# Optimization experiments

Measured on AMD Instinct MI355X. Metric: run time of the kernel, lower is better.

## Reference

```python
import jax, jax.numpy as jnp
import numpy as np

NUM_ITEMS = 50000
NUM_USERS = 16384   # static number of user segments (total_user universe)
H0 = 512            # encoder_hidden_size[0]
LAT = 256           # bottleneck (encoder_hidden_size[-1] / decoder_hidden_size[0])
N = 262144          # observed interactions
NT = 262144         # target interactions


def setup_inputs() -> dict:
    key = jax.random.key(0)
    ks = jax.random.split(key, 14)

    def glorot(k, shape):
        fan_in, fan_out = shape[1], shape[0]
        lim = np.sqrt(6.0 / (fan_in + fan_out)).astype(np.float32)
        return jax.random.uniform(k, shape, jnp.float32, -lim, lim)

    return {
        "user": jax.random.randint(ks[0], (N,), 0, NUM_USERS, jnp.int32),
        "item": jax.random.randint(ks[1], (N,), 0, NUM_ITEMS, jnp.int32),
        "rating": jax.random.normal(ks[2], (N,), jnp.float32),
        "target_user": jax.random.randint(ks[3], (NT,), 0, NUM_USERS, jnp.int32),
        "target_item": jax.random.randint(ks[4], (NT,), 0, NUM_ITEMS, jnp.int32),
        "target_rating": jax.random.normal(ks[5], (NT,), jnp.float32),
        # encoder_linear: Linear(num_items, H0)
        "W_enc": glorot(ks[6], (H0, NUM_ITEMS)),
        "b_enc": jnp.zeros((H0,), jnp.float32),
        # Encoder: Linear(H0, LAT) + Tanh
        "W1": glorot(ks[7], (LAT, H0)),
        "b1": jnp.zeros((LAT,), jnp.float32),
        # Decoder: Linear(LAT, H0) + Tanh
        "W2": glorot(ks[8], (H0, LAT)),
        "b2": jnp.zeros((H0,), jnp.float32),
        # decoder_linear: Linear(H0, num_items)
        "W_dec": glorot(ks[9], (NUM_ITEMS, H0)),
        "b_dec": jnp.zeros((NUM_ITEMS,), jnp.float32),
    }


def reference(user, item, rating, target_user, target_item, target_rating,
              W_enc, b_enc, W1, b1, W2, b2, W_dec, b_dec):
    # --- encoder: gather item weight rows, scale by rating, segment-sum per user ---
    # rows: [N, H0] gather from W_enc.T ([NUM_ITEMS, H0])
    rows = W_enc.T[item] * rating[:, None]
    # per-user aggregation over the full user universe (equivalent to the
    # torch unique/sort/index_add path: users with no interactions get 0 -> tanh(bias))
    agg = jax.ops.segment_sum(rows, user, num_segments=NUM_USERS)  # [U, H0]
    x = jnp.tanh(agg + b_enc)
    # --- small dense tanh MLP encoder/decoder ---
    encoded = jnp.tanh(x @ W1.T + b1)          # [U, LAT]
    decoded = jnp.tanh(encoded @ W2.T + b2)    # [U, H0] (dropout = identity, eval mode)
    # --- decoder: gather user codes & item decoder rows, rowwise dot ---
    g = decoded[target_user]                   # [NT, H0]
    w = W_dec[target_item]                     # [NT, H0]
    pred = jnp.sum(g * w, axis=-1) + b_dec[target_item]  # [NT]
    loss = jnp.mean((pred - target_rating) ** 2)
    return pred, loss
```

## Files before the change

kernel.cpp:

```cpp
#include <hip/hip_runtime.h>
#include <hip/hip_bf16.h>
#include <math.h>

#define NUM_ITEMS 50000
#define NUM_USERS 16384
#define ITEM_BINS 50176
#define H0 512
#define LAT 256

typedef __attribute__((ext_vector_type(8))) short short8;
typedef __attribute__((ext_vector_type(4))) float floatx4;

__device__ __forceinline__ unsigned short f2bf(float f) {
    union { float f; unsigned i; } u; u.f = f;
    unsigned r = u.i + 0x7fff + ((u.i >> 16) & 1);
    return (unsigned short)(r >> 16);
}
__device__ __forceinline__ float bfhi(unsigned v) {
    union { unsigned i; float f; } u; u.i = v & 0xffff0000u; return u.f;
}
__device__ __forceinline__ float bflo(unsigned v) {
    union { unsigned i; float f; } u; u.i = v << 16; return u.f;
}

__global__ void transpose_kernel(const float* __restrict__ src, unsigned short* __restrict__ dst) {
    __shared__ float tile[32][33];
    int tx = threadIdx.x, ty = threadIdx.y;
    int x0 = blockIdx.x * 32, y0 = blockIdx.y * 32;
    int x = x0 + tx;
    if (x < NUM_ITEMS) {
#pragma unroll
        for (int j = 0; j < 32; j += 8)
            tile[ty + j][tx] = src[(size_t)(y0 + ty + j) * NUM_ITEMS + x];
    }
    __syncthreads();
#pragma unroll
    for (int j = 0; j < 32; j += 8) {
        int it = x0 + ty + j;
        if (it < NUM_ITEMS)
            dst[(size_t)it * H0 + y0 + tx] = f2bf(tile[tx][ty + j]);
    }
}

__global__ void f2bf2_kernel(const float* __restrict__ a, unsigned short* __restrict__ da,
                             const float* __restrict__ b, unsigned short* __restrict__ db, int n) {
    int i = blockIdx.x * blockDim.x + threadIdx.x;
    if (i < n) da[i] = f2bf(a[i]);
    else { int j = i - n; if (j < n) db[j] = f2bf(b[j]); }
}

__global__ void count_kernel(const int* __restrict__ user, int* __restrict__ cntU,
                             const int* __restrict__ t_item, int* __restrict__ cntI,
                             int n, int nt) {
    int i = blockIdx.x * blockDim.x + threadIdx.x;
    if (i < n) atomicAdd(&cntU[user[i]], 1);
    if (i < nt) atomicAdd(&cntI[t_item[i]], 1);
}

__device__ void scan_block(const int* __restrict__ cnt, int* __restrict__ offs,
                           int* __restrict__ cursor, int per) {
    __shared__ int ssum[1024];
    int t = threadIdx.x;
    int base = t * per;
    int s = 0;
    for (int j = 0; j < per; ++j) s += cnt[base + j];
    ssum[t] = s;
    __syncthreads();
    for (int off = 1; off < 1024; off <<= 1) {
        int v = (t >= off) ? ssum[t - off] : 0;
        __syncthreads();
        ssum[t] += v;
        __syncthreads();
    }
    int run = (t == 0) ? 0 : ssum[t - 1];
    for (int j = 0; j < per; ++j) {
        offs[base + j] = run;
        cursor[base + j] = run;
        run += cnt[base + j];
    }
}

__global__ void scan_kernel(const int* __restrict__ cntU, int* __restrict__ offsU, int* __restrict__ curU,
                            const int* __restrict__ cntI, int* __restrict__ offsI, int* __restrict__ curI) {
    if (blockIdx.x == 0) scan_block(cntU, offsU, curU, NUM_USERS / 1024);
    else scan_block(cntI, offsI, curI, ITEM_BINS / 1024);
}

__global__ void scatter_kernel(const int* __restrict__ user, const int* __restrict__ item,
                               const float* __restrict__ rating, int* __restrict__ curU,
                               int* __restrict__ s_item, float* __restrict__ s_rat,
                               const int* __restrict__ t_user, const int* __restrict__ t_item,
                               const float* __restrict__ t_rating, int* __restrict__ curI,
                               int* __restrict__ st_user, int* __restrict__ st_item,
                               float* __restrict__ st_rat, int* __restrict__ st_idx,
                               int n, int nt) {
    int i = blockIdx.x * blockDim.x + threadIdx.x;
    if (i < n) {
        int u = user[i];
        int pos = atomicAdd(&curU[u], 1);
        s_item[pos] = item[i];
        s_rat[pos] = rating[i];
    }
    if (i < nt) {
        int it = t_item[i];
        int pos = atomicAdd(&curI[it], 1);
        st_user[pos] = t_user[i];
        st_item[pos] = it;
        st_rat[pos] = t_rating[i];
        st_idx[pos] = i;
    }
}

__global__ __launch_bounds__(256) void agg_kernel(const unsigned short* __restrict__ wtb,
                                                  const int* __restrict__ offs,
                                                  const int* __restrict__ ends,
                                                  const int* __restrict__ s_item,
                                                  const float* __restrict__ s_rat,
                                                  const float* __restrict__ b_enc,
                                                  unsigned short* __restrict__ xb) {
    __shared__ float red[3 * 512];
    int u = blockIdx.x;
    int tid = threadIdx.x;
    int g = tid >> 6, lane = tid & 63;
    float acc[8] = {};
    int j0 = offs[u], j1 = ends[u];
    for (int j = j0 + g; j < j1; j += 4) {
        int it = s_item[j];
        float r = s_rat[j];
        uint4 v = ((const uint4*)(wtb + (size_t)it * H0))[lane];
        acc[0] += bflo(v.x) * r; acc[1] += bfhi(v.x) * r;
        acc[2] += bflo(v.y) * r; acc[3] += bfhi(v.y) * r;
        acc[4] += bflo(v.z) * r; acc[5] += bfhi(v.z) * r;
        acc[6] += bflo(v.w) * r; acc[7] += bfhi(v.w) * r;
    }
    if (g) {
        float4* rp = (float4*)red + (size_t)(g - 1) * 128 + lane * 2;
        rp[0] = make_float4(acc[0], acc[1], acc[2], acc[3]);
        rp[1] = make_float4(acc[4], acc[5], acc[6], acc[7]);
    }
    __syncthreads();
    if (g == 0) {
#pragma unroll
        for (int h = 0; h < 3; ++h) {
            const float* rp = red + h * 512 + lane * 8;
#pragma unroll
            for (int e = 0; e < 8; ++e) acc[e] += rp[e];
        }
        float4 b0 = ((const float4*)b_enc)[lane * 2];
        float4 b1 = ((const float4*)b_enc)[lane * 2 + 1];
        unsigned short o[8];
        o[0] = f2bf(tanhf(acc[0] + b0.x)); o[1] = f2bf(tanhf(acc[1] + b0.y));
        o[2] = f2bf(tanhf(acc[2] + b0.z)); o[3] = f2bf(tanhf(acc[3] + b0.w));
        o[4] = f2bf(tanhf(acc[4] + b1.x)); o[5] = f2bf(tanhf(acc[5] + b1.y));
        o[6] = f2bf(tanhf(acc[6] + b1.z)); o[7] = f2bf(tanhf(acc[7] + b1.w));
        uint4 pk;
        pk.x = (unsigned)o[0] | ((unsigned)o[1] << 16);
        pk.y = (unsigned)o[2] | ((unsigned)o[3] << 16);
        pk.z = (unsigned)o[4] | ((unsigned)o[5] << 16);
        pk.w = (unsigned)o[6] | ((unsigned)o[7] << 16);
        ((uint4*)(xb + (size_t)u * H0))[lane] = pk;
    }
}

__global__ __launch_bounds__(256) void gemm_mfma(const unsigned short* __restrict__ A,
                                                 const unsigned short* __restrict__ B,
                                                 const float* __restrict__ bias,
                                                 unsigned short* __restrict__ C,
                                                 int Nn, int K) {
    __shared__ unsigned short Ash[128 * 32];
    __shared__ unsigned short Bsh[128 * 32];
    int tid = threadIdx.x;
    int wid = tid >> 6, lane = tid & 63;
    int wave_m = wid & 1, wave_n = wid >> 1;
    int quad = lane >> 4, l16 = lane & 15;
    int m0 = blockIdx.x * 128, n0 = blockIdx.y * 128;
    floatx4 acc[4][4] = {};

    int srow = lane >> 2;
    int scol = (lane & 3) * 8;
    for (int k0 = 0; k0 < K; k0 += 32) {
#pragma unroll
        for (int i = 0; i < 2; ++i) {
            int c = wid * 2 + i;
            int row = c * 16 + srow;
            const unsigned short* ga = A + (size_t)(m0 + row) * K + k0 + scol;
            const unsigned short* gb = B + (size_t)(n0 + row) * K + k0 + scol;
            __builtin_amdgcn_global_load_lds(
                (const __attribute__((address_space(1))) void*)ga,
                (__attribute__((address_space(3))) void*)((__attribute__((address_space(3))) char*)Ash + c * 1024),
                16, 0, 0);
            __builtin_amdgcn_global_load_lds(
                (const __attribute__((address_space(1))) void*)gb,
                (__attribute__((address_space(3))) void*)((__attribute__((address_space(3))) char*)Bsh + c * 1024),
                16, 0, 0);
        }
        __syncthreads();
        short8 af[4], bfr[4];
#pragma unroll
        for (int i = 0; i < 4; ++i) {
            int ml = wave_m * 64 + i * 16 + l16;
            af[i] = ((const short8*)Ash)[ml * 4 + quad];
            int nl = wave_n * 64 + i * 16 + l16;
            bfr[i] = ((const short8*)Bsh)[nl * 4 + quad];
        }
#pragma unroll
        for (int i = 0; i < 4; ++i)
#pragma unroll
            for (int j = 0; j < 4; ++j)
                acc[i][j] = __builtin_amdgcn_mfma_f32_16x16x32_bf16(af[i], bfr[j], acc[i][j], 0, 0, 0);
        __syncthreads();
    }
#pragma unroll
    for (int j = 0; j < 4; ++j) {
        int col = n0 + wave_n * 64 + j * 16 + l16;
        float bv = bias[col];
#pragma unroll
        for (int i = 0; i < 4; ++i) {
            int rowb = m0 + wave_m * 64 + i * 16 + quad * 4;
#pragma unroll
            for (int r = 0; r < 4; ++r)
                C[(size_t)(rowb + r) * Nn + col] = f2bf(tanhf(acc[i][j][r] + bv));
        }
    }
}

__global__ __launch_bounds__(256) void predict_kernel(const unsigned short* __restrict__ dec_b,
                                                      const float* __restrict__ W_dec,
                                                      const float* __restrict__ b_dec,
                                                      const int* __restrict__ st_user,
                                                      const int* __restrict__ st_item,
                                                      const float* __restrict__ st_rat,
                                                      const int* __restrict__ st_idx,
                                                      float* __restrict__ pred,
                                                      float* __restrict__ partials, int NT) {
    __shared__ float wsum[4];
    int wid = threadIdx.x >> 6, lane = threadIdx.x & 63;
    int base = (blockIdx.x * 4 + wid) * 4;
    float sq = 0.f;
    int tu[4], ti[4];
    uint4 gv[4];
    float4 wv0[4], wv1[4];
#pragma unroll
    for (int t = 0; t < 4; ++t) {
        int idx = min(base + t, NT - 1);
        tu[t] = st_user[idx];
        ti[t] = st_item[idx];
    }
#pragma unroll
    for (int t = 0; t < 4; ++t) {
        gv[t] = ((const uint4*)(dec_b + (size_t)tu[t] * H0))[lane];
        const float4* w = (const float4*)(W_dec + (size_t)ti[t] * H0);
        wv0[t] = w[lane * 2];
        wv1[t] = w[lane * 2 + 1];
    }
#pragma unroll
    for (int t = 0; t < 4; ++t) {
        float s = bflo(gv[t].x) * wv0[t].x + bfhi(gv[t].x) * wv0[t].y
                + bflo(gv[t].y) * wv0[t].z + bfhi(gv[t].y) * wv0[t].w
                + bflo(gv[t].z) * wv1[t].x + bfhi(gv[t].z) * wv1[t].y
                + bflo(gv[t].w) * wv1[t].z + bfhi(gv[t].w) * wv1[t].w;
#pragma unroll
        for (int off = 32; off; off >>= 1) s += __shfl_xor(s, off, 64);
        if (lane == 0 && base + t < NT) {
            int idx = base + t;
            float p = s + b_dec[ti[t]];
            pred[st_idx[idx]] = p;
            float d = p - st_rat[idx];
            sq += d * d;
        }
    }
    if (lane == 0) wsum[wid] = sq;
    __syncthreads();
    if (threadIdx.x == 0) partials[blockIdx.x] = wsum[0] + wsum[1] + wsum[2] + wsum[3];
}

__global__ void loss_reduce(const float* __restrict__ partials, float* __restrict__ out_loss,
                            int nPart, float invNT) {
    __shared__ float s[256];
    int t = threadIdx.x;
    float a = 0.f;
    for (int i = t; i < nPart; i += 256) a += partials[i];
    s[t] = a;
    __syncthreads();
    for (int off = 128; off; off >>= 1) {
        if (t < off) s[t] += s[t + off];
        __syncthreads();
    }
    if (t == 0) out_loss[0] = s[0] * invNT;
}

extern "C" void kernel_launch(void* const* d_in, const int* in_sizes, int n_in,
                              void* d_out, int out_size, void* d_ws, size_t ws_size,
                              hipStream_t stream) {
    const int* user = (const int*)d_in[0];
    const int* item = (const int*)d_in[1];
    const float* rating = (const float*)d_in[2];
    const int* t_user = (const int*)d_in[3];
    const int* t_item = (const int*)d_in[4];
    const float* t_rating = (const float*)d_in[5];
    const float* W_enc = (const float*)d_in[6];
    const float* b_enc = (const float*)d_in[7];
    const float* W1 = (const float*)d_in[8];
    const float* b1 = (const float*)d_in[9];
    const float* W2 = (const float*)d_in[10];
    const float* b2 = (const float*)d_in[11];
    const float* W_dec = (const float*)d_in[12];
    const float* b_dec = (const float*)d_in[13];
    const int N = in_sizes[0];
    const int NT = in_sizes[3];

    char* ws = (char*)d_ws;
    size_t off = 0;
    auto alloc = [&](size_t bytes) {
        void* p = ws + off;
        off = (off + bytes + 255) & ~(size_t)255;
        return p;
    };
    unsigned short* wtb = (unsigned short*)alloc((size_t)NUM_ITEMS * H0 * 2);
    unsigned short* xb = (unsigned short*)alloc((size_t)NUM_USERS * H0 * 2);
    unsigned short* enc_b = (unsigned short*)alloc((size_t)NUM_USERS * LAT * 2);
    unsigned short* dec_b = (unsigned short*)alloc((size_t)NUM_USERS * H0 * 2);
    unsigned short* w1b = (unsigned short*)alloc((size_t)LAT * H0 * 2);
    unsigned short* w2b = (unsigned short*)alloc((size_t)H0 * LAT * 2);
    int* cntU = (int*)alloc((size_t)(NUM_USERS + ITEM_BINS) * 4);
    int* cntI = cntU + NUM_USERS;
    int* offsU = (int*)alloc((size_t)NUM_USERS * 4);
    int* curU = (int*)alloc((size_t)NUM_USERS * 4);
    int* offsI = (int*)alloc((size_t)ITEM_BINS * 4);
    int* curI = (int*)alloc((size_t)ITEM_BINS * 4);
    int* s_item = (int*)alloc((size_t)N * 4);
    float* s_rat = (float*)alloc((size_t)N * 4);
    int* st_user = (int*)alloc((size_t)NT * 4);
    int* st_item = (int*)alloc((size_t)NT * 4);
    float* st_rat = (float*)alloc((size_t)NT * 4);
    int* st_idx = (int*)alloc((size_t)NT * 4);
    const int predBlocks = (NT + 15) / 16;
    float* partials = (float*)alloc((size_t)predBlocks * 4);

    float* pred = (float*)d_out;
    float* loss = pred + NT;

    const int maxNNT = N > NT ? N : NT;
    hipMemsetAsync(cntU, 0, (size_t)(NUM_USERS + ITEM_BINS) * 4, stream);
    count_kernel<<<(maxNNT + 255) / 256, 256, 0, stream>>>(user, cntU, t_item, cntI, N, NT);
    scan_kernel<<<2, 1024, 0, stream>>>(cntU, offsU, curU, cntI, offsI, curI);
    scatter_kernel<<<(maxNNT + 255) / 256, 256, 0, stream>>>(
        user, item, rating, curU, s_item, s_rat,
        t_user, t_item, t_rating, curI, st_user, st_item, st_rat, st_idx, N, NT);
    transpose_kernel<<<dim3((NUM_ITEMS + 31) / 32, H0 / 32), dim3(32, 8), 0, stream>>>(W_enc, wtb);
    f2bf2_kernel<<<(2 * LAT * H0 + 255) / 256, 256, 0, stream>>>(W1, w1b, W2, w2b, LAT * H0);
    agg_kernel<<<NUM_USERS, 256, 0, stream>>>(wtb, offsU, curU, s_item, s_rat, b_enc, xb);
    gemm_mfma<<<dim3(NUM_USERS / 128, LAT / 128), 256, 0, stream>>>(xb, w1b, b1, enc_b, LAT, H0);
    gemm_mfma<<<dim3(NUM_USERS / 128, H0 / 128), 256, 0, stream>>>(enc_b, w2b, b2, dec_b, H0, LAT);
    predict_kernel<<<predBlocks, 256, 0, stream>>>(dec_b, W_dec, b_dec, st_user, st_item, st_rat,
                                                   st_idx, pred, partials, NT);
    loss_reduce<<<1, 256, 0, stream>>>(partials, loss, predBlocks, 1.0f / NT);
}
```

Before: 472.8 us.

## Fuse setup kernels, pack sorted records, convert W_dec to bf16, shrink GEMM tile

Merges the W_enc transpose, weight conversions and counting into one multi-role setup kernel with wider 64x64 transpose tiles and vectorized count loads. Sorted interaction and target records are packed into int2/int4 structs so each needs one load, and the agg loop prefetches the next record. W_dec is converted to bf16 up front so predict gathers half the bytes, at the cost of a full extra streaming pass over W_dec and lower precision in the dot product. The GEMM is templated to a 128x64 tile for more blocks, and the scan and loss reduce use vector loads.

```diff
diff --git a/kernel.cpp b/kernel.cpp
--- a/kernel.cpp
+++ b/kernel.cpp
@@ -4,7 +4,7 @@
 
 #define NUM_ITEMS 50000
 #define NUM_USERS 16384
-#define ITEM_BINS 50176
+#define ITEM_BINS 65536
 #define H0 512
 #define LAT 256
 
@@ -22,39 +22,76 @@
 __device__ __forceinline__ float bflo(unsigned v) {
     union { unsigned i; float f; } u; u.i = v << 16; return u.f;
 }
-
-__global__ void transpose_kernel(const float* __restrict__ src, unsigned short* __restrict__ dst) {
-    __shared__ float tile[32][33];
-    int tx = threadIdx.x, ty = threadIdx.y;
-    int x0 = blockIdx.x * 32, y0 = blockIdx.y * 32;
-    int x = x0 + tx;
-    if (x < NUM_ITEMS) {
-#pragma unroll
-        for (int j = 0; j < 32; j += 8)
-            tile[ty + j][tx] = src[(size_t)(y0 + ty + j) * NUM_ITEMS + x];
-    }
-    __syncthreads();
-#pragma unroll
-    for (int j = 0; j < 32; j += 8) {
-        int it = x0 + ty + j;
-        if (it < NUM_ITEMS)
-            dst[(size_t)it * H0 + y0 + tx] = f2bf(tile[tx][ty + j]);
-    }
-}
-
-__global__ void f2bf2_kernel(const float* __restrict__ a, unsigned short* __restrict__ da,
-                             const float* __restrict__ b, unsigned short* __restrict__ db, int n) {
-    int i = blockIdx.x * blockDim.x + threadIdx.x;
-    if (i < n) da[i] = f2bf(a[i]);
-    else { int j = i - n; if (j < n) db[j] = f2bf(b[j]); }
-}
-
-__global__ void count_kernel(const int* __restrict__ user, int* __restrict__ cntU,
-                             const int* __restrict__ t_item, int* __restrict__ cntI,
-                             int n, int nt) {
-    int i = blockIdx.x * blockDim.x + threadIdx.x;
-    if (i < n) atomicAdd(&cntU[user[i]], 1);
-    if (i < nt) atomicAdd(&cntI[t_item[i]], 1);
+__device__ __forceinline__ uint4 pack8(const float* v) {
+    uint4 p;
+    p.x = (unsigned)f2bf(v[0]) | ((unsigned)f2bf(v[1]) << 16);
+    p.y = (unsigned)f2bf(v[2]) | ((unsigned)f2bf(v[3]) << 16);
+    p.z = (unsigned)f2bf(v[4]) | ((unsigned)f2bf(v[5]) << 16);
+    p.w = (unsigned)f2bf(v[6]) | ((unsigned)f2bf(v[7]) << 16);
+    return p;
+}
+
+__global__ __launch_bounds__(256) void setup_kernel(
+        const float* __restrict__ W_enc, unsigned short* __restrict__ wtb,
+        const float* __restrict__ W_dec, unsigned short* __restrict__ wdb,
+        const float* __restrict__ W1, unsigned short* __restrict__ w1b,
+        const float* __restrict__ W2, unsigned short* __restrict__ w2b,
+        const int* __restrict__ user, int* __restrict__ cntU,
+        const int* __restrict__ t_item, int* __restrict__ cntI,
+        int n, int nt, int TB, int DB, int CB) {
+    __shared__ float tile[64][65];
+    int bid = blockIdx.x;
+    int tid = threadIdx.x;
+    if (bid < TB) {
+        const int TBX = (NUM_ITEMS + 63) / 64;
+        int bx = bid % TBX, by = bid / TBX;
+        int x0 = bx * 64, y0 = by * 64;
+        int tx = tid & 63, ty = tid >> 6;
+        int x = x0 + tx;
+        if (x < NUM_ITEMS) {
+#pragma unroll
+            for (int j = 0; j < 64; j += 4)
+                tile[j + ty][tx] = W_enc[(size_t)(y0 + j + ty) * NUM_ITEMS + x];
+        }
+        __syncthreads();
+#pragma unroll
+        for (int j = 0; j < 64; j += 4) {
+            int it = x0 + j + ty;
+            if (it < NUM_ITEMS)
+                wtb[(size_t)it * H0 + y0 + tx] = f2bf(tile[tx][j + ty]);
+        }
+    } else if (bid < TB + DB) {
+        int idx = (bid - TB) * 2048 + tid * 8;
+        float v[8];
+        *(float4*)&v[0] = *(const float4*)(W_dec + idx);
+        *(float4*)&v[4] = *(const float4*)(W_dec + idx + 4);
+        *(uint4*)(wdb + idx) = pack8(v);
+    } else if (bid < TB + DB + CB) {
+        int i = (bid - TB - DB) * 1024 + tid * 4;
+        if (i + 3 < n) {
+            int4 u = *(const int4*)(user + i);
+            atomicAdd(&cntU[u.x], 1); atomicAdd(&cntU[u.y], 1);
+            atomicAdd(&cntU[u.z], 1); atomicAdd(&cntU[u.w], 1);
+        } else {
+            for (int k = i; k < n; ++k) atomicAdd(&cntU[user[k]], 1);
+        }
+        if (i + 3 < nt) {
+            int4 t = *(const int4*)(t_item + i);
+            atomicAdd(&cntI[t.x], 1); atomicAdd(&cntI[t.y], 1);
+            atomicAdd(&cntI[t.z], 1); atomicAdd(&cntI[t.w], 1);
+        } else {
+            for (int k = i; k < nt; ++k) atomicAdd(&cntI[t_item[k]], 1);
+        }
+    } else {
+        int b2i = bid - TB - DB - CB;
+        const float* src = (b2i < 64) ? W1 : W2;
+        unsigned short* dst = (b2i < 64) ? w1b : w2b;
+        int idx = (b2i & 63) * 2048 + tid * 8;
+        float v[8];
+        *(float4*)&v[0] = *(const float4*)(src + idx);
+        *(float4*)&v[4] = *(const float4*)(src + idx + 4);
+        *(uint4*)(dst + idx) = pack8(v);
+    }
 }
 
 __device__ void scan_block(const int* __restrict__ cnt, int* __restrict__ offs,
@@ -63,7 +100,10 @@
     int t = threadIdx.x;
     int base = t * per;
     int s = 0;
-    for (int j = 0; j < per; ++j) s += cnt[base + j];
+    for (int j = 0; j < per; j += 4) {
+        int4 v = *(const int4*)(cnt + base + j);
+        s += v.x + v.y + v.z + v.w;
+    }
     ssum[t] = s;
     __syncthreads();
     for (int off = 1; off < 1024; off <<= 1) {
@@ -73,10 +113,15 @@
         __syncthreads();
     }
     int run = (t == 0) ? 0 : ssum[t - 1];
-    for (int j = 0; j < per; ++j) {
-        offs[base + j] = run;
-        cursor[base + j] = run;
-        run += cnt[base + j];
+    for (int j = 0; j < per; j += 4) {
+        int4 v = *(const int4*)(cnt + base + j);
+        int4 o;
+        o.x = run; run += v.x;
+        o.y = run; run += v.y;
+        o.z = run; run += v.z;
+        o.w = run; run += v.w;
+        *(int4*)(offs + base + j) = o;
+        *(int4*)(cursor + base + j) = o;
     }
 }
 
@@ -88,34 +133,27 @@
 
 __global__ void scatter_kernel(const int* __restrict__ user, const int* __restrict__ item,
                                const float* __restrict__ rating, int* __restrict__ curU,
-                               int* __restrict__ s_item, float* __restrict__ s_rat,
+                               int2* __restrict__ s_pack,
                                const int* __restrict__ t_user, const int* __restrict__ t_item,
                                const float* __restrict__ t_rating, int* __restrict__ curI,
-                               int* __restrict__ st_user, int* __restrict__ st_item,
-                               float* __restrict__ st_rat, int* __restrict__ st_idx,
-                               int n, int nt) {
+                               int4* __restrict__ st_pack, int n, int nt) {
     int i = blockIdx.x * blockDim.x + threadIdx.x;
     if (i < n) {
         int u = user[i];
         int pos = atomicAdd(&curU[u], 1);
-        s_item[pos] = item[i];
-        s_rat[pos] = rating[i];
+        s_pack[pos] = make_int2(item[i], __float_as_int(rating[i]));
     }
     if (i < nt) {
         int it = t_item[i];
         int pos = atomicAdd(&curI[it], 1);
-        st_user[pos] = t_user[i];
-        st_item[pos] = it;
-        st_rat[pos] = t_rating[i];
-        st_idx[pos] = i;
+        st_pack[pos] = make_int4(t_user[i], it, __float_as_int(t_rating[i]), i);
     }
 }
 
 __global__ __launch_bounds__(256) void agg_kernel(const unsigned short* __restrict__ wtb,
                                                   const int* __restrict__ offs,
                                                   const int* __restrict__ ends,
-                                                  const int* __restrict__ s_item,
-                                                  const float* __restrict__ s_rat,
+                                                  const int2* __restrict__ s_pack,
                                                   const float* __restrict__ b_enc,
                                                   unsigned short* __restrict__ xb) {
     __shared__ float red[3 * 512];
@@ -124,14 +162,19 @@
     int g = tid >> 6, lane = tid & 63;
     float acc[8] = {};
     int j0 = offs[u], j1 = ends[u];
-    for (int j = j0 + g; j < j1; j += 4) {
-        int it = s_item[j];
-        float r = s_rat[j];
-        uint4 v = ((const uint4*)(wtb + (size_t)it * H0))[lane];
+    int j = j0 + g;
+    int2 nxt = (j < j1) ? s_pack[j] : make_int2(0, 0);
+    while (j < j1) {
+        int2 cur = nxt;
+        int jn = j + 4;
+        if (jn < j1) nxt = s_pack[jn];
+        float r = __int_as_float(cur.y);
+        uint4 v = ((const uint4*)(wtb + (size_t)cur.x * H0))[lane];
         acc[0] += bflo(v.x) * r; acc[1] += bfhi(v.x) * r;
         acc[2] += bflo(v.y) * r; acc[3] += bfhi(v.y) * r;
         acc[4] += bflo(v.z) * r; acc[5] += bfhi(v.z) * r;
         acc[6] += bflo(v.w) * r; acc[7] += bfhi(v.w) * r;
+        j = jn;
     }
     if (g) {
         float4* rp = (float4*)red + (size_t)(g - 1) * 128 + lane * 2;
@@ -148,71 +191,74 @@
         }
         float4 b0 = ((const float4*)b_enc)[lane * 2];
         float4 b1 = ((const float4*)b_enc)[lane * 2 + 1];
-        unsigned short o[8];
-        o[0] = f2bf(tanhf(acc[0] + b0.x)); o[1] = f2bf(tanhf(acc[1] + b0.y));
-        o[2] = f2bf(tanhf(acc[2] + b0.z)); o[3] = f2bf(tanhf(acc[3] + b0.w));
-        o[4] = f2bf(tanhf(acc[4] + b1.x)); o[5] = f2bf(tanhf(acc[5] + b1.y));
-        o[6] = f2bf(tanhf(acc[6] + b1.z)); o[7] = f2bf(tanhf(acc[7] + b1.w));
-        uint4 pk;
-        pk.x = (unsigned)o[0] | ((unsigned)o[1] << 16);
-        pk.y = (unsigned)o[2] | ((unsigned)o[3] << 16);
-        pk.z = (unsigned)o[4] | ((unsigned)o[5] << 16);
-        pk.w = (unsigned)o[6] | ((unsigned)o[7] << 16);
-        ((uint4*)(xb + (size_t)u * H0))[lane] = pk;
-    }
-}
-
+        float o[8];
+        o[0] = tanhf(acc[0] + b0.x); o[1] = tanhf(acc[1] + b0.y);
+        o[2] = tanhf(acc[2] + b0.z); o[3] = tanhf(acc[3] + b0.w);
+        o[4] = tanhf(acc[4] + b1.x); o[5] = tanhf(acc[5] + b1.y);
+        o[6] = tanhf(acc[6] + b1.z); o[7] = tanhf(acc[7] + b1.w);
+        ((uint4*)(xb + (size_t)u * H0))[lane] = pack8(o);
+    }
+}
+
+template<int BN>
 __global__ __launch_bounds__(256) void gemm_mfma(const unsigned short* __restrict__ A,
                                                  const unsigned short* __restrict__ B,
                                                  const float* __restrict__ bias,
                                                  unsigned short* __restrict__ C,
                                                  int Nn, int K) {
+    constexpr int WN = BN / 32;
+    constexpr int NCH = 8 + BN / 16;
+    constexpr int PER = NCH / 4;
     __shared__ unsigned short Ash[128 * 32];
-    __shared__ unsigned short Bsh[128 * 32];
+    __shared__ unsigned short Bsh[BN * 32];
     int tid = threadIdx.x;
     int wid = tid >> 6, lane = tid & 63;
     int wave_m = wid & 1, wave_n = wid >> 1;
     int quad = lane >> 4, l16 = lane & 15;
-    int m0 = blockIdx.x * 128, n0 = blockIdx.y * 128;
-    floatx4 acc[4][4] = {};
-
+    int m0 = blockIdx.x * 128, n0 = blockIdx.y * BN;
+    floatx4 acc[4][WN] = {};
     int srow = lane >> 2;
     int scol = (lane & 3) * 8;
     for (int k0 = 0; k0 < K; k0 += 32) {
 #pragma unroll
-        for (int i = 0; i < 2; ++i) {
-            int c = wid * 2 + i;
-            int row = c * 16 + srow;
-            const unsigned short* ga = A + (size_t)(m0 + row) * K + k0 + scol;
-            const unsigned short* gb = B + (size_t)(n0 + row) * K + k0 + scol;
-            __builtin_amdgcn_global_load_lds(
-                (const __attribute__((address_space(1))) void*)ga,
-                (__attribute__((address_space(3))) void*)((__attribute__((address_space(3))) char*)Ash + c * 1024),
-                16, 0, 0);
-            __builtin_amdgcn_global_load_lds(
-                (const __attribute__((address_space(1))) void*)gb,
-                (__attribute__((address_space(3))) void*)((__attribute__((address_space(3))) char*)Bsh + c * 1024),
-                16, 0, 0);
-        }
-        __syncthreads();
-        short8 af[4], bfr[4];
+        for (int i = 0; i < PER; ++i) {
+            int c = wid * PER + i;
+            if (c < 8) {
+                const unsigned short* ga = A + (size_t)(m0 + c * 16 + srow) * K + k0 + scol;
+                __builtin_amdgcn_global_load_lds(
+                    (const __attribute__((address_space(1))) void*)ga,
+                    (__attribute__((address_space(3))) void*)((__attribute__((address_space(3))) char*)Ash + c * 1024),
+                    16, 0, 0);
+            } else {
+                const unsigned short* gb = B + (size_t)(n0 + (c - 8) * 16 + srow) * K + k0 + scol;
+                __builtin_amdgcn_global_load_lds(
+                    (const __attribute__((address_space(1))) void*)gb,
+                    (__attribute__((address_space(3))) void*)((__attribute__((address_space(3))) char*)Bsh + (c - 8) * 1024),
+                    16, 0, 0);
+            }
+        }
+        __syncthreads();
+        short8 af[4], bfr[WN];
 #pragma unroll
         for (int i = 0; i < 4; ++i) {
             int ml = wave_m * 64 + i * 16 + l16;
             af[i] = ((const short8*)Ash)[ml * 4 + quad];
-            int nl = wave_n * 64 + i * 16 + l16;
-            bfr[i] = ((const short8*)Bsh)[nl * 4 + quad];
+        }
+#pragma unroll
+        for (int j = 0; j < WN; ++j) {
+            int nl = wave_n * (BN / 2) + j * 16 + l16;
+            bfr[j] = ((const short8*)Bsh)[nl * 4 + quad];
         }
 #pragma unroll
         for (int i = 0; i < 4; ++i)
 #pragma unroll
-            for (int j = 0; j < 4; ++j)
+            for (int j = 0; j < WN; ++j)
                 acc[i][j] = __builtin_amdgcn_mfma_f32_16x16x32_bf16(af[i], bfr[j], acc[i][j], 0, 0, 0);
         __syncthreads();
     }
 #pragma unroll
-    for (int j = 0; j < 4; ++j) {
-        int col = n0 + wave_n * 64 + j * 16 + l16;
+    for (int j = 0; j < WN; ++j) {
+        int col = n0 + wave_n * (BN / 2) + j * 16 + l16;
         float bv = bias[col];
 #pragma unroll
         for (int i = 0; i < 4; ++i) {
@@ -225,47 +271,36 @@
 }
 
 __global__ __launch_bounds__(256) void predict_kernel(const unsigned short* __restrict__ dec_b,
-                                                      const float* __restrict__ W_dec,
+                                                      const unsigned short* __restrict__ wdb,
                                                       const float* __restrict__ b_dec,
-                                                      const int* __restrict__ st_user,
-                                                      const int* __restrict__ st_item,
-                                                      const float* __restrict__ st_rat,
-                                                      const int* __restrict__ st_idx,
+                                                      const int4* __restrict__ st,
                                                       float* __restrict__ pred,
                                                       float* __restrict__ partials, int NT) {
     __shared__ float wsum[4];
     int wid = threadIdx.x >> 6, lane = threadIdx.x & 63;
     int base = (blockIdx.x * 4 + wid) * 4;
     float sq = 0.f;
-    int tu[4], ti[4];
-    uint4 gv[4];
-    float4 wv0[4], wv1[4];
+    int4 tv[4];
+    uint4 gv[4], wv[4];
+#pragma unroll
+    for (int t = 0; t < 4; ++t) tv[t] = st[min(base + t, NT - 1)];
 #pragma unroll
     for (int t = 0; t < 4; ++t) {
-        int idx = min(base + t, NT - 1);
-        tu[t] = st_user[idx];
-        ti[t] = st_item[idx];
+        gv[t] = ((const uint4*)(dec_b + (size_t)tv[t].x * H0))[lane];
+        wv[t] = ((const uint4*)(wdb + (size_t)tv[t].y * H0))[lane];
     }
 #pragma unroll
     for (int t = 0; t < 4; ++t) {
-        gv[t] = ((const uint4*)(dec_b + (size_t)tu[t] * H0))[lane];
-        const float4* w = (const float4*)(W_dec + (size_t)ti[t] * H0);
-        wv0[t] = w[lane * 2];
-        wv1[t] = w[lane * 2 + 1];
-    }
-#pragma unroll
-    for (int t = 0; t < 4; ++t) {
-        float s = bflo(gv[t].x) * wv0[t].x + bfhi(gv[t].x) * wv0[t].y
-                + bflo(gv[t].y) * wv0[t].z + bfhi(gv[t].y) * wv0[t].w
-                + bflo(gv[t].z) * wv1[t].x + bfhi(gv[t].z) * wv1[t].y
-                + bflo(gv[t].w) * wv1[t].z + bfhi(gv[t].w) * wv1[t].w;
+        float s = bflo(gv[t].x) * bflo(wv[t].x) + bfhi(gv[t].x) * bfhi(wv[t].x)
+                + bflo(gv[t].y) * bflo(wv[t].y) + bfhi(gv[t].y) * bfhi(wv[t].y)
+                + bflo(gv[t].z) * bflo(wv[t].z) + bfhi(gv[t].z) * bfhi(wv[t].z)
+                + bflo(gv[t].w) * bflo(wv[t].w) + bfhi(gv[t].w) * bfhi(wv[t].w);
 #pragma unroll
         for (int off = 32; off; off >>= 1) s += __shfl_xor(s, off, 64);
         if (lane == 0 && base + t < NT) {
-            int idx = base + t;
-            float p = s + b_dec[ti[t]];
-            pred[st_idx[idx]] = p;
-            float d = p - st_rat[idx];
+            float p = s + b_dec[tv[t].y];
+            pred[tv[t].w] = p;
+            float d = p - __int_as_float(tv[t].z);
             sq += d * d;
         }
     }
@@ -279,7 +314,13 @@
     __shared__ float s[256];
     int t = threadIdx.x;
     float a = 0.f;
-    for (int i = t; i < nPart; i += 256) a += partials[i];
+    const float4* p4 = (const float4*)partials;
+    int n4 = nPart >> 2;
+    for (int i = t; i < n4; i += 256) {
+        float4 v = p4[i];
+        a += v.x + v.y + v.z + v.w;
+    }
+    for (int i = (n4 << 2) + t; i < nPart; i += 256) a += partials[i];
     s[t] = a;
     __syncthreads();
     for (int off = 128; off; off >>= 1) {
@@ -317,6 +358,7 @@
         return p;
     };
     unsigned short* wtb = (unsigned short*)alloc((size_t)NUM_ITEMS * H0 * 2);
+    unsigned short* wdb = (unsigned short*)alloc((size_t)NUM_ITEMS * H0 * 2);
     unsigned short* xb = (unsigned short*)alloc((size_t)NUM_USERS * H0 * 2);
     unsigned short* enc_b = (unsigned short*)alloc((size_t)NUM_USERS * LAT * 2);
     unsigned short* dec_b = (unsigned short*)alloc((size_t)NUM_USERS * H0 * 2);
@@ -328,12 +370,8 @@
     int* curU = (int*)alloc((size_t)NUM_USERS * 4);
     int* offsI = (int*)alloc((size_t)ITEM_BINS * 4);
     int* curI = (int*)alloc((size_t)ITEM_BINS * 4);
-    int* s_item = (int*)alloc((size_t)N * 4);
-    float* s_rat = (float*)alloc((size_t)N * 4);
-    int* st_user = (int*)alloc((size_t)NT * 4);
-    int* st_item = (int*)alloc((size_t)NT * 4);
-    float* st_rat = (float*)alloc((size_t)NT * 4);
-    int* st_idx = (int*)alloc((size_t)NT * 4);
+    int2* s_pack = (int2*)alloc((size_t)N * 8);
+    int4* st_pack = (int4*)alloc((size_t)NT * 16);
     const int predBlocks = (NT + 15) / 16;
     float* partials = (float*)alloc((size_t)predBlocks * 4);
 
@@ -341,18 +379,23 @@
     float* loss = pred + NT;
 
     const int maxNNT = N > NT ? N : NT;
+    const int TBX = (NUM_ITEMS + 63) / 64;
+    const int TB = TBX * (H0 / 64);
+    const int DB = (NUM_ITEMS * H0) / 2048;
+    const int CB = (maxNNT + 1023) / 1024;
+    const int WB = 128;
+
     hipMemsetAsync(cntU, 0, (size_t)(NUM_USERS + ITEM_BINS) * 4, stream);
-    count_kernel<<<(maxNNT + 255) / 256, 256, 0, stream>>>(user, cntU, t_item, cntI, N, NT);
+    setup_kernel<<<TB + DB + CB + WB, 256, 0, stream>>>(
+        W_enc, wtb, W_dec, wdb, W1, w1b, W2, w2b,
+        user, cntU, t_item, cntI, N, NT, TB, DB, CB);
     scan_kernel<<<2, 1024, 0, stream>>>(cntU, offsU, curU, cntI, offsI, curI);
     scatter_kernel<<<(maxNNT + 255) / 256, 256, 0, stream>>>(
-        user, item, rating, curU, s_item, s_rat,
-        t_user, t_item, t_rating, curI, st_user, st_item, st_rat, st_idx, N, NT);
-    transpose_kernel<<<dim3((NUM_ITEMS + 31) / 32, H0 / 32), dim3(32, 8), 0, stream>>>(W_enc, wtb);
-    f2bf2_kernel<<<(2 * LAT * H0 + 255) / 256, 256, 0, stream>>>(W1, w1b, W2, w2b, LAT * H0);
-    agg_kernel<<<NUM_USERS, 256, 0, stream>>>(wtb, offsU, curU, s_item, s_rat, b_enc, xb);
-    gemm_mfma<<<dim3(NUM_USERS / 128, LAT / 128), 256, 0, stream>>>(xb, w1b, b1, enc_b, LAT, H0);
-    gemm_mfma<<<dim3(NUM_USERS / 128, H0 / 128), 256, 0, stream>>>(enc_b, w2b, b2, dec_b, H0, LAT);
-    predict_kernel<<<predBlocks, 256, 0, stream>>>(dec_b, W_dec, b_dec, st_user, st_item, st_rat,
-                                                   st_idx, pred, partials, NT);
+        user, item, rating, curU, s_pack,
+        t_user, t_item, t_rating, curI, st_pack, N, NT);
+    agg_kernel<<<NUM_USERS, 256, 0, stream>>>(wtb, offsU, curU, s_pack, b_enc, xb);
+    gemm_mfma<64><<<dim3(NUM_USERS / 128, LAT / 64), 256, 0, stream>>>(xb, w1b, b1, enc_b, LAT, H0);
+    gemm_mfma<64><<<dim3(NUM_USERS / 128, H0 / 64), 256, 0, stream>>>(enc_b, w2b, b2, dec_b, H0, LAT);
+    predict_kernel<<<predBlocks, 256, 0, stream>>>(dec_b, wdb, b_dec, st_pack, pred, partials, NT);
     loss_reduce<<<1, 256, 0, stream>>>(partials, loss, predBlocks, 1.0f / NT);
 }
```

New measurement: 463.4 us. 2.0% less time.
